# Optimization experiments

Hardware: AMD Instinct MI355X
Metric: run time of the kernel (lower is better)

The kernel has to match this reference:

```python
import jax, jax.numpy as jnp
import numpy as np

B, C, H, W = 1024, 1024, 14, 14
A = 8          # adt_num (number of expert branches)
CH = C // 4    # expert bottleneck width


def setup_inputs() -> dict:
    key = jax.random.key(0)
    ks = jax.random.split(key, 5)
    s_in = 1.0 / np.sqrt(C)
    s_hid = 1.0 / np.sqrt(CH)
    return {
        "features": jax.random.normal(ks[0], (B, C, H, W), dtype=jnp.float32),
        "fc_w": jax.random.normal(ks[1], (A, C), dtype=jnp.float32) * s_in,
        "fc_b": jnp.zeros((A,), dtype=jnp.float32),
        "fc1_w": jax.random.normal(ks[2], (A, C, CH), dtype=jnp.float32) * s_in,
        "fc1_b": jnp.zeros((A, CH), dtype=jnp.float32),
        "fc2_w": jax.random.normal(ks[3], (A, CH, C), dtype=jnp.float32) * s_hid,
        "fc2_b": jnp.zeros((A, C), dtype=jnp.float32),
    }


def reference(features, fc_w, fc_b, fc1_w, fc1_b, fc2_w, fc2_b):
    # Global average pool over spatial dims: [B, C]
    pooled = jnp.mean(features.reshape(features.shape[0], features.shape[1], -1), axis=2)
    # All adt_num expert branches as one batched GEMM pair: [B, A, CH] -> [B, A, C]
    h = jax.nn.relu(jnp.einsum("bc,ach->bah", pooled, fc1_w) + fc1_b)
    expert = jnp.einsum("bah,ahc->bac", h, fc2_w) + fc2_b
    # Softmax gating over experts: [B, A]
    gate = jax.nn.softmax(pooled @ fc_w.T + fc_b, axis=1)
    # Gate-weighted sum of expert outputs: [B, C]
    mixed = jnp.einsum("ba,bac->bc", gate, expert)
    # Sigmoid channel gate + residual: out = x * sigmoid(mixed) + x
    scale = jax.nn.sigmoid(mixed)[:, :, None, None]
    return features * scale + features
```

## Files before the change

### kernel.cpp

```cpp
#include <hip/hip_runtime.h>

#define B_  1024
#define C_  1024
#define HW_ 196
#define A_  8
#define CH_ 256
#define N1_ 2048
#define K2_ 2048

typedef __attribute__((ext_vector_type(8))) short short8;
typedef __attribute__((ext_vector_type(4))) float f32x4;

#define KT1 32
#define KT2 64

static __device__ __forceinline__ unsigned short f2bf(float x) {
  union { float f; unsigned u; } v; v.f = x;
  unsigned r = (v.u + 0x7FFFu + ((v.u >> 16) & 1u)) >> 16;
  return (unsigned short)r;
}

__global__ __launch_bounds__(256) void pooltc_k(const float* __restrict__ f,
                                                float* __restrict__ pooled,
                                                const float* __restrict__ fc1_w,
                                                const float* __restrict__ fc2_w,
                                                unsigned short* __restrict__ w1t,
                                                unsigned short* __restrict__ w2t) {
  __shared__ float tile[32][33];
  if (blockIdx.x < 4096) {
    unsigned row = blockIdx.x * 256 + threadIdx.x;
    const f32x4* p = (const f32x4*)f + (size_t)row * 49;
    float s = 0.f;
    #pragma unroll 3
    for (int j = 0; j < 12; ++j) {
      f32x4 a = p[4 * j + 0], b = p[4 * j + 1], c = p[4 * j + 2], d = p[4 * j + 3];
      s += (a.x + a.y) + (a.z + a.w);
      s += (b.x + b.y) + (b.z + b.w);
      s += (c.x + c.y) + (c.z + c.w);
      s += (d.x + d.y) + (d.z + d.w);
    }
    f32x4 e = p[48];
    s += (e.x + e.y) + (e.z + e.w);
    pooled[row] = s * (1.0f / 196.0f);
  } else {
    int t = blockIdx.x - 4096;
    const float* in; unsigned short* outb; int Cc, nt0, kt, KT;
    if (t < 2048) {
      int a = t >> 8, rem = t & 255;
      int c0 = (rem & 7) * 32, k0 = (rem >> 3) * 32;
      in  = fc1_w + (size_t)a * (C_ * CH_) + (size_t)k0 * CH_ + c0;
      Cc = CH_;
      nt0 = a * 16 + (c0 >> 4);  kt = k0 >> 5;  KT = KT1;  outb = w1t;
    } else {
      t -= 2048;
      int a = t >> 8, rem = t & 255;
      int c0 = (rem & 31) * 32, ch0 = (rem >> 5) * 32;
      in  = fc2_w + (size_t)a * (CH_ * C_) + (size_t)ch0 * C_ + c0;
      Cc = C_;
      nt0 = c0 >> 4;  kt = a * 8 + (ch0 >> 5);  KT = KT2;  outb = w2t;
    }
    int tx = threadIdx.x & 31, ty = threadIdx.x >> 5;
    #pragma unroll
    for (int i = 0; i < 32; i += 8)
      tile[ty + i][tx] = in[(size_t)(ty + i) * Cc + tx];
    __syncthreads();
    int tt = threadIdx.x;
    if (tt < 128) {
      int ct = tt >> 6, kg = (tt >> 4) & 3, r = tt & 15;
      short8 v;
      #pragma unroll
      for (int j = 0; j < 8; ++j)
        v[j] = (short)f2bf(tile[kg * 8 + j][ct * 16 + r]);
      size_t base = ((size_t)(nt0 + ct) * KT + kt) * 512 + (size_t)(kg * 16 + r) * 8;
      *(short8*)(outb + base) = v;
    }
  }
}

__global__ void gate_k(const float* __restrict__ pooled, const float* __restrict__ fc_w,
                       const float* __restrict__ fc_b, float* __restrict__ gate,
                       unsigned short* __restrict__ a1t) {
  __shared__ float dots[A_];
  if (blockIdx.x < 1024) {
    int b = blockIdx.x;
    int wave = threadIdx.x >> 6, lane = threadIdx.x & 63;
    const float* p = pooled + (size_t)b * C_;
    for (int e = wave; e < A_; e += 4) {
      const float* wrow = fc_w + (size_t)e * C_;
      float sum = 0.f;
      for (int c = lane; c < C_; c += 64) sum += p[c] * wrow[c];
      #pragma unroll
      for (int off = 32; off > 0; off >>= 1) sum += __shfl_down(sum, off, 64);
      if (lane == 0) dots[e] = sum + fc_b[e];
    }
    __syncthreads();
    if (threadIdx.x == 0) {
      float mx = dots[0];
      for (int e = 1; e < A_; ++e) mx = fmaxf(mx, dots[e]);
      float ex[A_], se = 0.f;
      for (int e = 0; e < A_; ++e) { ex[e] = __expf(dots[e] - mx); se += ex[e]; }
      float inv = 1.0f / se;
      for (int e = 0; e < A_; ++e) gate[(size_t)b * A_ + e] = ex[e] * inv;
    }
  } else {
    int h = blockIdx.x - 1024;
    int rt = h >> 1, kt0 = (h & 1) * 16;
    int t = threadIdx.x;
    int e0 = 2 * t;
    int kg = e0 >> 7, r = (e0 >> 3) & 15, j0 = e0 & 7;
    int row = rt * 16 + r;
    for (int kt = kt0; kt < kt0 + 16; ++kt) {
      int col = kt * 32 + kg * 8 + j0;
      float v0 = pooled[(size_t)row * C_ + col];
      float v1 = pooled[(size_t)row * C_ + col + 1];
      size_t base = ((size_t)rt * KT1 + kt) * 512 + e0;
      a1t[base]     = f2bf(v0);
      a1t[base + 1] = f2bf(v1);
    }
  }
}

__global__ __launch_bounds__(256) void gemm1_k(const unsigned short* __restrict__ A1,
                                               const unsigned short* __restrict__ W1,
                                               const float* __restrict__ fc1_b,
                                               const float* __restrict__ gate,
                                               unsigned short* __restrict__ gh) {
  int w = threadIdx.x >> 6, lane = threadIdx.x & 63;
  int rt0 = blockIdx.x * 4 + (w >> 1) * 2;
  int nt0 = blockIdx.y * 4 + (w & 1) * 2;
  const short8* Ap0 = (const short8*)(A1 + (size_t)(rt0    ) * KT1 * 512 + lane * 8);
  const short8* Ap1 = (const short8*)(A1 + (size_t)(rt0 + 1) * KT1 * 512 + lane * 8);
  const short8* Bp0 = (const short8*)(W1 + (size_t)(nt0    ) * KT1 * 512 + lane * 8);
  const short8* Bp1 = (const short8*)(W1 + (size_t)(nt0 + 1) * KT1 * 512 + lane * 8);
  f32x4 acc[2][2];
  acc[0][0] = (f32x4){0,0,0,0}; acc[0][1] = acc[0][0];
  acc[1][0] = acc[0][0];        acc[1][1] = acc[0][0];
  #pragma unroll 4
  for (int kt = 0; kt < KT1; ++kt) {
    short8 a0 = Ap0[64 * kt], a1 = Ap1[64 * kt];
    short8 b0 = Bp0[64 * kt], b1 = Bp1[64 * kt];
    acc[0][0] = __builtin_amdgcn_mfma_f32_16x16x32_bf16(a0, b0, acc[0][0], 0, 0, 0);
    acc[0][1] = __builtin_amdgcn_mfma_f32_16x16x32_bf16(a0, b1, acc[0][1], 0, 0, 0);
    acc[1][0] = __builtin_amdgcn_mfma_f32_16x16x32_bf16(a1, b0, acc[1][0], 0, 0, 0);
    acc[1][1] = __builtin_amdgcn_mfma_f32_16x16x32_bf16(a1, b1, acc[1][1], 0, 0, 0);
  }
  int r = lane & 15, kg = lane >> 4;
  #pragma unroll
  for (int mi = 0; mi < 2; ++mi)
    #pragma unroll
    for (int ni = 0; ni < 2; ++ni) {
      int col = (nt0 + ni) * 16 + r;
      float bias = fc1_b[col];
      int aidx = col >> 8;
      #pragma unroll
      for (int reg = 0; reg < 4; ++reg) {
        int row = (rt0 + mi) * 16 + kg * 4 + reg;
        float val = acc[mi][ni][reg] + bias;
        val = fmaxf(val, 0.f) * gate[row * A_ + aidx];
        size_t idx = ((size_t)(row >> 4) * KT2 + (col >> 5)) * 512
                   + (size_t)((col >> 3) & 3) * 128 + (size_t)(row & 15) * 8 + (col & 7);
        gh[idx] = f2bf(val);
      }
    }
}

__global__ __launch_bounds__(256) void gemm2_k(const unsigned short* __restrict__ GH,
                                               const unsigned short* __restrict__ W2,
                                               const float* __restrict__ gate,
                                               const float* __restrict__ fc2_b,
                                               float* __restrict__ s_out) {
  int w = threadIdx.x >> 6, lane = threadIdx.x & 63;
  int rt0 = blockIdx.x * 4 + (w >> 1) * 2;
  int nt0 = blockIdx.y * 4 + (w & 1) * 2;
  const short8* Ap0 = (const short8*)(GH + (size_t)(rt0    ) * KT2 * 512 + lane * 8);
  const short8* Ap1 = (const short8*)(GH + (size_t)(rt0 + 1) * KT2 * 512 + lane * 8);
  const short8* Bp0 = (const short8*)(W2 + (size_t)(nt0    ) * KT2 * 512 + lane * 8);
  const short8* Bp1 = (const short8*)(W2 + (size_t)(nt0 + 1) * KT2 * 512 + lane * 8);
  f32x4 acc[2][2];
  acc[0][0] = (f32x4){0,0,0,0}; acc[0][1] = acc[0][0];
  acc[1][0] = acc[0][0];        acc[1][1] = acc[0][0];
  #pragma unroll 4
  for (int kt = 0; kt < KT2; ++kt) {
    short8 a0 = Ap0[64 * kt], a1 = Ap1[64 * kt];
    short8 b0 = Bp0[64 * kt], b1 = Bp1[64 * kt];
    acc[0][0] = __builtin_amdgcn_mfma_f32_16x16x32_bf16(a0, b0, acc[0][0], 0, 0, 0);
    acc[0][1] = __builtin_amdgcn_mfma_f32_16x16x32_bf16(a0, b1, acc[0][1], 0, 0, 0);
    acc[1][0] = __builtin_amdgcn_mfma_f32_16x16x32_bf16(a1, b0, acc[1][0], 0, 0, 0);
    acc[1][1] = __builtin_amdgcn_mfma_f32_16x16x32_bf16(a1, b1, acc[1][1], 0, 0, 0);
  }
  int r = lane & 15, kg = lane >> 4;
  #pragma unroll
  for (int mi = 0; mi < 2; ++mi)
    #pragma unroll
    for (int ni = 0; ni < 2; ++ni) {
      int col = (nt0 + ni) * 16 + r;
      float b8[A_];
      #pragma unroll
      for (int a = 0; a < A_; ++a) b8[a] = fc2_b[a * C_ + col];
      #pragma unroll
      for (int reg = 0; reg < 4; ++reg) {
        int row = (rt0 + mi) * 16 + kg * 4 + reg;
        const float* g = gate + (size_t)row * A_;
        float bias = 0.f;
        #pragma unroll
        for (int a = 0; a < A_; ++a) bias += g[a] * b8[a];
        float mixed = acc[mi][ni][reg] + bias;
        s_out[(size_t)row * C_ + col] = 1.0f + 1.0f / (1.0f + __expf(-mixed));
      }
    }
}

__global__ __launch_bounds__(256) void apply_k(const f32x4* __restrict__ f,
                                               const float* __restrict__ s,
                                               f32x4* __restrict__ out, unsigned total4) {
  unsigned i = blockIdx.x * 256 + threadIdx.x;
  unsigned stride = gridDim.x * 256;
  for (; i < total4; i += stride) {
    f32x4 v = __builtin_nontemporal_load(&f[i]);
    float m = s[i / 49u];
    v *= m;
    __builtin_nontemporal_store(v, &out[i]);
  }
}

extern "C" void kernel_launch(void* const* d_in, const int* in_sizes, int n_in,
                              void* d_out, int out_size, void* d_ws, size_t ws_size,
                              hipStream_t stream) {
  const float* features = (const float*)d_in[0];
  const float* fc_w  = (const float*)d_in[1];
  const float* fc_b  = (const float*)d_in[2];
  const float* fc1_w = (const float*)d_in[3];
  const float* fc1_b = (const float*)d_in[4];
  const float* fc2_w = (const float*)d_in[5];
  const float* fc2_b = (const float*)d_in[6];
  float* out = (float*)d_out;
  char* ws = (char*)d_ws;

  float*          pooled = (float*)(ws);
  unsigned short* a1t    = (unsigned short*)(ws + 0x400000);
  float*          gate   = (float*)(ws + 0x600000);
  unsigned short* gh     = (unsigned short*)(ws + 0x610000);
  unsigned short* w1t    = (unsigned short*)(ws + 0xA10000);
  unsigned short* w2t    = (unsigned short*)(ws + 0xE10000);
  float*          s_buf  = (float*)(ws + 0x1210000);

  pooltc_k<<<8192, 256, 0, stream>>>(features, pooled, fc1_w, fc2_w, w1t, w2t);
  gate_k<<<1152, 256, 0, stream>>>(pooled, fc_w, fc_b, gate, a1t);
  gemm1_k<<<dim3(16, 32), 256, 0, stream>>>(a1t, w1t, fc1_b, gate, gh);
  gemm2_k<<<dim3(16, 16), 256, 0, stream>>>(gh, w2t, gate, fc2_b, s_buf);
  apply_k<<<8192, 256, 0, stream>>>((const f32x4*)features, s_buf, (f32x4*)out,
                                    (unsigned)(out_size / 4));
}
```

Baseline: 515.0 us.

## Fuse all stages into one persistent kernel with software grid barriers

Replaces five kernel launches with one persistent kernel of 512 blocks that separates the stages (pool and weight transpose, gating, GEMM1, GEMM2, apply) with atomic-counter grid barriers. The bf16 A-operand layout for GEMM1 is now written directly during pooling, which removes the separate a1t repack pass. The aim is to cut launch gaps and tail effects between stages. In exchange, each stage runs with only 512 blocks, so the streaming pool and apply phases have less latency hiding, and the barriers depend on every block being co-resident.

Result: slower. 1.039 ms (+101.7%).

```diff
diff --git a/kernel.cpp b/kernel.cpp
--- a/kernel.cpp
+++ b/kernel.cpp
@@ -2,17 +2,14 @@
 
 #define B_  1024
 #define C_  1024
-#define HW_ 196
 #define A_  8
 #define CH_ 256
-#define N1_ 2048
-#define K2_ 2048
+#define KT1 32
+#define KT2 64
+#define G_  512
 
 typedef __attribute__((ext_vector_type(8))) short short8;
 typedef __attribute__((ext_vector_type(4))) float f32x4;
-
-#define KT1 32
-#define KT2 64
 
 static __device__ __forceinline__ unsigned short f2bf(float x) {
   union { float f; unsigned u; } v; v.f = x;
@@ -20,70 +17,99 @@
   return (unsigned short)r;
 }
 
-__global__ __launch_bounds__(256) void pooltc_k(const float* __restrict__ f,
-                                                float* __restrict__ pooled,
-                                                const float* __restrict__ fc1_w,
-                                                const float* __restrict__ fc2_w,
-                                                unsigned short* __restrict__ w1t,
-                                                unsigned short* __restrict__ w2t) {
+__device__ unsigned long long g_bar[4];
+
+static __device__ __forceinline__ void gridbar(int slot) {
+  __syncthreads();
+  if (threadIdx.x == 0) {
+    __threadfence();
+    unsigned long long v = __hip_atomic_fetch_add(&g_bar[slot], 1ull,
+                              __ATOMIC_ACQ_REL, __HIP_MEMORY_SCOPE_AGENT) + 1ull;
+    unsigned long long tgt = ((v + (unsigned long long)(G_ - 1)) /
+                              (unsigned long long)G_) * (unsigned long long)G_;
+    while (__hip_atomic_load(&g_bar[slot], __ATOMIC_ACQUIRE,
+                             __HIP_MEMORY_SCOPE_AGENT) < tgt)
+      __builtin_amdgcn_s_sleep(2);
+    __threadfence();
+  }
+  __syncthreads();
+}
+
+
+__global__ __launch_bounds__(256, 2) void fused_k(
+    const float* __restrict__ features,
+    const float* __restrict__ fc_w,  const float* __restrict__ fc_b,
+    const float* __restrict__ fc1_w, const float* __restrict__ fc1_b,
+    const float* __restrict__ fc2_w, const float* __restrict__ fc2_b,
+    float* __restrict__ out,
+    float* __restrict__ pooled, unsigned short* __restrict__ a1t,
+    float* __restrict__ gate,   unsigned short* __restrict__ gh,
+    unsigned short* __restrict__ w1t, unsigned short* __restrict__ w2t,
+    float* __restrict__ s_buf) {
   __shared__ float tile[32][33];
-  if (blockIdx.x < 4096) {
-    unsigned row = blockIdx.x * 256 + threadIdx.x;
-    const f32x4* p = (const f32x4*)f + (size_t)row * 49;
-    float s = 0.f;
-    #pragma unroll 3
-    for (int j = 0; j < 12; ++j) {
-      f32x4 a = p[4 * j + 0], b = p[4 * j + 1], c = p[4 * j + 2], d = p[4 * j + 3];
-      s += (a.x + a.y) + (a.z + a.w);
-      s += (b.x + b.y) + (b.z + b.w);
-      s += (c.x + c.y) + (c.z + c.w);
-      s += (d.x + d.y) + (d.z + d.w);
-    }
-    f32x4 e = p[48];
-    s += (e.x + e.y) + (e.z + e.w);
-    pooled[row] = s * (1.0f / 196.0f);
-  } else {
-    int t = blockIdx.x - 4096;
-    const float* in; unsigned short* outb; int Cc, nt0, kt, KT;
-    if (t < 2048) {
-      int a = t >> 8, rem = t & 255;
-      int c0 = (rem & 7) * 32, k0 = (rem >> 3) * 32;
-      in  = fc1_w + (size_t)a * (C_ * CH_) + (size_t)k0 * CH_ + c0;
-      Cc = CH_;
-      nt0 = a * 16 + (c0 >> 4);  kt = k0 >> 5;  KT = KT1;  outb = w1t;
+  __shared__ float dots[A_];
+  const int bid = blockIdx.x;
+  const int tid = threadIdx.x;
+
+  for (int u = bid; u < 8192; u += G_) {
+    if (u < 4096) {
+      unsigned rowf = (unsigned)u * 256 + tid;
+      const f32x4* p = (const f32x4*)features + (size_t)rowf * 49;
+      float s = 0.f;
+      #pragma unroll 3
+      for (int j = 0; j < 12; ++j) {
+        f32x4 a = p[4 * j + 0], b = p[4 * j + 1], c = p[4 * j + 2], d = p[4 * j + 3];
+        s += (a.x + a.y) + (a.z + a.w);
+        s += (b.x + b.y) + (b.z + b.w);
+        s += (c.x + c.y) + (c.z + c.w);
+        s += (d.x + d.y) + (d.z + d.w);
+      }
+      f32x4 e = p[48];
+      s += (e.x + e.y) + (e.z + e.w);
+      float m = s * (1.0f / 196.0f);
+      pooled[rowf] = m;
+      int b = rowf >> 10, c = rowf & 1023;
+      size_t idx = ((size_t)(b >> 4) * KT1 + (c >> 5)) * 512
+                 + (size_t)((c >> 3) & 3) * 128 + (size_t)(b & 15) * 8 + (c & 7);
+      a1t[idx] = f2bf(m);
     } else {
-      t -= 2048;
-      int a = t >> 8, rem = t & 255;
-      int c0 = (rem & 31) * 32, ch0 = (rem >> 5) * 32;
-      in  = fc2_w + (size_t)a * (CH_ * C_) + (size_t)ch0 * C_ + c0;
-      Cc = C_;
-      nt0 = c0 >> 4;  kt = a * 8 + (ch0 >> 5);  KT = KT2;  outb = w2t;
-    }
-    int tx = threadIdx.x & 31, ty = threadIdx.x >> 5;
-    #pragma unroll
-    for (int i = 0; i < 32; i += 8)
-      tile[ty + i][tx] = in[(size_t)(ty + i) * Cc + tx];
-    __syncthreads();
-    int tt = threadIdx.x;
-    if (tt < 128) {
-      int ct = tt >> 6, kg = (tt >> 4) & 3, r = tt & 15;
-      short8 v;
-      #pragma unroll
-      for (int j = 0; j < 8; ++j)
-        v[j] = (short)f2bf(tile[kg * 8 + j][ct * 16 + r]);
-      size_t base = ((size_t)(nt0 + ct) * KT + kt) * 512 + (size_t)(kg * 16 + r) * 8;
-      *(short8*)(outb + base) = v;
-    }
-  }
-}
-
-__global__ void gate_k(const float* __restrict__ pooled, const float* __restrict__ fc_w,
-                       const float* __restrict__ fc_b, float* __restrict__ gate,
-                       unsigned short* __restrict__ a1t) {
-  __shared__ float dots[A_];
-  if (blockIdx.x < 1024) {
-    int b = blockIdx.x;
-    int wave = threadIdx.x >> 6, lane = threadIdx.x & 63;
+      int t = u - 4096;
+      const float* in; unsigned short* outb; int Cc, nt0, kt, KT;
+      if (t < 2048) {
+        int a = t >> 8, rem = t & 255;
+        int c0 = (rem & 7) * 32, k0 = (rem >> 3) * 32;
+        in  = fc1_w + (size_t)a * (C_ * CH_) + (size_t)k0 * CH_ + c0;
+        Cc = CH_;
+        nt0 = a * 16 + (c0 >> 4);  kt = k0 >> 5;  KT = KT1;  outb = w1t;
+      } else {
+        t -= 2048;
+        int a = t >> 8, rem = t & 255;
+        int c0 = (rem & 31) * 32, ch0 = (rem >> 5) * 32;
+        in  = fc2_w + (size_t)a * (CH_ * C_) + (size_t)ch0 * C_ + c0;
+        Cc = C_;
+        nt0 = c0 >> 4;  kt = a * 8 + (ch0 >> 5);  KT = KT2;  outb = w2t;
+      }
+      int tx = tid & 31, ty = tid >> 5;
+      #pragma unroll
+      for (int i = 0; i < 32; i += 8)
+        tile[ty + i][tx] = in[(size_t)(ty + i) * Cc + tx];
+      __syncthreads();
+      if (tid < 128) {
+        int ct = tid >> 6, kg = (tid >> 4) & 3, r = tid & 15;
+        short8 v;
+        #pragma unroll
+        for (int j = 0; j < 8; ++j)
+          v[j] = (short)f2bf(tile[kg * 8 + j][ct * 16 + r]);
+        size_t base = ((size_t)(nt0 + ct) * KT + kt) * 512 + (size_t)(kg * 16 + r) * 8;
+        *(short8*)(outb + base) = v;
+      }
+      __syncthreads();
+    }
+  }
+  gridbar(0);
+
+  for (int b = bid; b < B_; b += G_) {
+    int wave = tid >> 6, lane = tid & 63;
     const float* p = pooled + (size_t)b * C_;
     for (int e = wave; e < A_; e += 4) {
       const float* wrow = fc_w + (size_t)e * C_;
@@ -94,7 +120,7 @@
       if (lane == 0) dots[e] = sum + fc_b[e];
     }
     __syncthreads();
-    if (threadIdx.x == 0) {
+    if (tid == 0) {
       float mx = dots[0];
       for (int e = 1; e < A_; ++e) mx = fmaxf(mx, dots[e]);
       float ex[A_], se = 0.f;
@@ -102,124 +128,114 @@
       float inv = 1.0f / se;
       for (int e = 0; e < A_; ++e) gate[(size_t)b * A_ + e] = ex[e] * inv;
     }
-  } else {
-    int h = blockIdx.x - 1024;
-    int rt = h >> 1, kt0 = (h & 1) * 16;
-    int t = threadIdx.x;
-    int e0 = 2 * t;
-    int kg = e0 >> 7, r = (e0 >> 3) & 15, j0 = e0 & 7;
-    int row = rt * 16 + r;
-    for (int kt = kt0; kt < kt0 + 16; ++kt) {
-      int col = kt * 32 + kg * 8 + j0;
-      float v0 = pooled[(size_t)row * C_ + col];
-      float v1 = pooled[(size_t)row * C_ + col + 1];
-      size_t base = ((size_t)rt * KT1 + kt) * 512 + e0;
-      a1t[base]     = f2bf(v0);
-      a1t[base + 1] = f2bf(v1);
-    }
-  }
-}
-
-__global__ __launch_bounds__(256) void gemm1_k(const unsigned short* __restrict__ A1,
-                                               const unsigned short* __restrict__ W1,
-                                               const float* __restrict__ fc1_b,
-                                               const float* __restrict__ gate,
-                                               unsigned short* __restrict__ gh) {
-  int w = threadIdx.x >> 6, lane = threadIdx.x & 63;
-  int rt0 = blockIdx.x * 4 + (w >> 1) * 2;
-  int nt0 = blockIdx.y * 4 + (w & 1) * 2;
-  const short8* Ap0 = (const short8*)(A1 + (size_t)(rt0    ) * KT1 * 512 + lane * 8);
-  const short8* Ap1 = (const short8*)(A1 + (size_t)(rt0 + 1) * KT1 * 512 + lane * 8);
-  const short8* Bp0 = (const short8*)(W1 + (size_t)(nt0    ) * KT1 * 512 + lane * 8);
-  const short8* Bp1 = (const short8*)(W1 + (size_t)(nt0 + 1) * KT1 * 512 + lane * 8);
-  f32x4 acc[2][2];
-  acc[0][0] = (f32x4){0,0,0,0}; acc[0][1] = acc[0][0];
-  acc[1][0] = acc[0][0];        acc[1][1] = acc[0][0];
-  #pragma unroll 4
-  for (int kt = 0; kt < KT1; ++kt) {
-    short8 a0 = Ap0[64 * kt], a1 = Ap1[64 * kt];
-    short8 b0 = Bp0[64 * kt], b1 = Bp1[64 * kt];
-    acc[0][0] = __builtin_amdgcn_mfma_f32_16x16x32_bf16(a0, b0, acc[0][0], 0, 0, 0);
-    acc[0][1] = __builtin_amdgcn_mfma_f32_16x16x32_bf16(a0, b1, acc[0][1], 0, 0, 0);
-    acc[1][0] = __builtin_amdgcn_mfma_f32_16x16x32_bf16(a1, b0, acc[1][0], 0, 0, 0);
-    acc[1][1] = __builtin_amdgcn_mfma_f32_16x16x32_bf16(a1, b1, acc[1][1], 0, 0, 0);
-  }
-  int r = lane & 15, kg = lane >> 4;
-  #pragma unroll
-  for (int mi = 0; mi < 2; ++mi)
+    __syncthreads();
+  }
+  gridbar(1);
+
+  {
+    int bx = bid >> 5, by = bid & 31;
+    int w = tid >> 6, lane = tid & 63;
+    int rt0 = bx * 4 + (w >> 1) * 2;
+    int nt0 = by * 4 + (w & 1) * 2;
+    const short8* Ap0 = (const short8*)(a1t + (size_t)(rt0    ) * KT1 * 512 + lane * 8);
+    const short8* Ap1 = (const short8*)(a1t + (size_t)(rt0 + 1) * KT1 * 512 + lane * 8);
+    const short8* Bp0 = (const short8*)(w1t + (size_t)(nt0    ) * KT1 * 512 + lane * 8);
+    const short8* Bp1 = (const short8*)(w1t + (size_t)(nt0 + 1) * KT1 * 512 + lane * 8);
+    f32x4 acc[2][2];
+    acc[0][0] = (f32x4){0,0,0,0}; acc[0][1] = acc[0][0];
+    acc[1][0] = acc[0][0];        acc[1][1] = acc[0][0];
+    #pragma unroll 4
+    for (int kt = 0; kt < KT1; ++kt) {
+      short8 a0 = Ap0[64 * kt], a1 = Ap1[64 * kt];
+      short8 b0 = Bp0[64 * kt], b1 = Bp1[64 * kt];
+      acc[0][0] = __builtin_amdgcn_mfma_f32_16x16x32_bf16(a0, b0, acc[0][0], 0, 0, 0);
+      acc[0][1] = __builtin_amdgcn_mfma_f32_16x16x32_bf16(a0, b1, acc[0][1], 0, 0, 0);
+      acc[1][0] = __builtin_amdgcn_mfma_f32_16x16x32_bf16(a1, b0, acc[1][0], 0, 0, 0);
+      acc[1][1] = __builtin_amdgcn_mfma_f32_16x16x32_bf16(a1, b1, acc[1][1], 0, 0, 0);
+    }
+    int r = lane & 15, kg = lane >> 4;
     #pragma unroll
-    for (int ni = 0; ni < 2; ++ni) {
-      int col = (nt0 + ni) * 16 + r;
-      float bias = fc1_b[col];
-      int aidx = col >> 8;
-      #pragma unroll
-      for (int reg = 0; reg < 4; ++reg) {
-        int row = (rt0 + mi) * 16 + kg * 4 + reg;
-        float val = acc[mi][ni][reg] + bias;
-        val = fmaxf(val, 0.f) * gate[row * A_ + aidx];
-        size_t idx = ((size_t)(row >> 4) * KT2 + (col >> 5)) * 512
-                   + (size_t)((col >> 3) & 3) * 128 + (size_t)(row & 15) * 8 + (col & 7);
-        gh[idx] = f2bf(val);
-      }
-    }
-}
-
-__global__ __launch_bounds__(256) void gemm2_k(const unsigned short* __restrict__ GH,
-                                               const unsigned short* __restrict__ W2,
-                                               const float* __restrict__ gate,
-                                               const float* __restrict__ fc2_b,
-                                               float* __restrict__ s_out) {
-  int w = threadIdx.x >> 6, lane = threadIdx.x & 63;
-  int rt0 = blockIdx.x * 4 + (w >> 1) * 2;
-  int nt0 = blockIdx.y * 4 + (w & 1) * 2;
-  const short8* Ap0 = (const short8*)(GH + (size_t)(rt0    ) * KT2 * 512 + lane * 8);
-  const short8* Ap1 = (const short8*)(GH + (size_t)(rt0 + 1) * KT2 * 512 + lane * 8);
-  const short8* Bp0 = (const short8*)(W2 + (size_t)(nt0    ) * KT2 * 512 + lane * 8);
-  const short8* Bp1 = (const short8*)(W2 + (size_t)(nt0 + 1) * KT2 * 512 + lane * 8);
-  f32x4 acc[2][2];
-  acc[0][0] = (f32x4){0,0,0,0}; acc[0][1] = acc[0][0];
-  acc[1][0] = acc[0][0];        acc[1][1] = acc[0][0];
-  #pragma unroll 4
-  for (int kt = 0; kt < KT2; ++kt) {
-    short8 a0 = Ap0[64 * kt], a1 = Ap1[64 * kt];
-    short8 b0 = Bp0[64 * kt], b1 = Bp1[64 * kt];
-    acc[0][0] = __builtin_amdgcn_mfma_f32_16x16x32_bf16(a0, b0, acc[0][0], 0, 0, 0);
-    acc[0][1] = __builtin_amdgcn_mfma_f32_16x16x32_bf16(a0, b1, acc[0][1], 0, 0, 0);
-    acc[1][0] = __builtin_amdgcn_mfma_f32_16x16x32_bf16(a1, b0, acc[1][0], 0, 0, 0);
-    acc[1][1] = __builtin_amdgcn_mfma_f32_16x16x32_bf16(a1, b1, acc[1][1], 0, 0, 0);
-  }
-  int r = lane & 15, kg = lane >> 4;
-  #pragma unroll
-  for (int mi = 0; mi < 2; ++mi)
+    for (int mi = 0; mi < 2; ++mi)
+      #pragma unroll
+      for (int ni = 0; ni < 2; ++ni) {
+        int col = (nt0 + ni) * 16 + r;
+        float bias = fc1_b[col];
+        int aidx = col >> 8;
+        #pragma unroll
+        for (int reg = 0; reg < 4; ++reg) {
+          int row = (rt0 + mi) * 16 + kg * 4 + reg;
+          float val = acc[mi][ni][reg] + bias;
+          val = fmaxf(val, 0.f) * gate[row * A_ + aidx];
+          size_t idx = ((size_t)(row >> 4) * KT2 + (col >> 5)) * 512
+                     + (size_t)((col >> 3) & 3) * 128 + (size_t)(row & 15) * 8 + (col & 7);
+          gh[idx] = f2bf(val);
+        }
+      }
+  }
+  gridbar(2);
+
+  if (bid < 256) {
+    int bx = bid >> 4, by = bid & 15;
+    int w = tid >> 6, lane = tid & 63;
+    int rt0 = bx * 4 + (w >> 1) * 2;
+    int nt0 = by * 4 + (w & 1) * 2;
+    const short8* Ap0 = (const short8*)(gh  + (size_t)(rt0    ) * KT2 * 512 + lane * 8);
+    const short8* Ap1 = (const short8*)(gh  + (size_t)(rt0 + 1) * KT2 * 512 + lane * 8);
+    const short8* Bp0 = (const short8*)(w2t + (size_t)(nt0    ) * KT2 * 512 + lane * 8);
+    const short8* Bp1 = (const short8*)(w2t + (size_t)(nt0 + 1) * KT2 * 512 + lane * 8);
+    f32x4 acc[2][2];
+    acc[0][0] = (f32x4){0,0,0,0}; acc[0][1] = acc[0][0];
+    acc[1][0] = acc[0][0];        acc[1][1] = acc[0][0];
+    #pragma unroll 4
+    for (int kt = 0; kt < KT2; ++kt) {
+      short8 a0 = Ap0[64 * kt], a1 = Ap1[64 * kt];
+      short8 b0 = Bp0[64 * kt], b1 = Bp1[64 * kt];
+      acc[0][0] = __builtin_amdgcn_mfma_f32_16x16x32_bf16(a0, b0, acc[0][0], 0, 0, 0);
+      acc[0][1] = __builtin_amdgcn_mfma_f32_16x16x32_bf16(a0, b1, acc[0][1], 0, 0, 0);
+      acc[1][0] = __builtin_amdgcn_mfma_f32_16x16x32_bf16(a1, b0, acc[1][0], 0, 0, 0);
+      acc[1][1] = __builtin_amdgcn_mfma_f32_16x16x32_bf16(a1, b1, acc[1][1], 0, 0, 0);
+    }
+    int r = lane & 15, kg = lane >> 4;
     #pragma unroll
-    for (int ni = 0; ni < 2; ++ni) {
-      int col = (nt0 + ni) * 16 + r;
-      float b8[A_];
-      #pragma unroll
-      for (int a = 0; a < A_; ++a) b8[a] = fc2_b[a * C_ + col];
-      #pragma unroll
-      for (int reg = 0; reg < 4; ++reg) {
-        int row = (rt0 + mi) * 16 + kg * 4 + reg;
-        const float* g = gate + (size_t)row * A_;
-        float bias = 0.f;
-        #pragma unroll
-        for (int a = 0; a < A_; ++a) bias += g[a] * b8[a];
-        float mixed = acc[mi][ni][reg] + bias;
-        s_out[(size_t)row * C_ + col] = 1.0f + 1.0f / (1.0f + __expf(-mixed));
-      }
-    }
-}
-
-__global__ __launch_bounds__(256) void apply_k(const f32x4* __restrict__ f,
-                                               const float* __restrict__ s,
-                                               f32x4* __restrict__ out, unsigned total4) {
-  unsigned i = blockIdx.x * 256 + threadIdx.x;
-  unsigned stride = gridDim.x * 256;
-  for (; i < total4; i += stride) {
-    f32x4 v = __builtin_nontemporal_load(&f[i]);
-    float m = s[i / 49u];
-    v *= m;
-    __builtin_nontemporal_store(v, &out[i]);
+    for (int mi = 0; mi < 2; ++mi)
+      #pragma unroll
+      for (int ni = 0; ni < 2; ++ni) {
+        int col = (nt0 + ni) * 16 + r;
+        float b8[A_];
+        #pragma unroll
+        for (int a = 0; a < A_; ++a) b8[a] = fc2_b[a * C_ + col];
+        #pragma unroll
+        for (int reg = 0; reg < 4; ++reg) {
+          int row = (rt0 + mi) * 16 + kg * 4 + reg;
+          const float* g = gate + (size_t)row * A_;
+          float bias = 0.f;
+          #pragma unroll
+          for (int a = 0; a < A_; ++a) bias += g[a] * b8[a];
+          float mixed = acc[mi][ni][reg] + bias;
+          s_buf[(size_t)row * C_ + col] = 1.0f + 1.0f / (1.0f + __expf(-mixed));
+        }
+      }
+  }
+  gridbar(3);
+
+  {
+    const f32x4* fv = (const f32x4*)features;
+    f32x4* ov = (f32x4*)out;
+    const unsigned stride = G_ * 256;
+    unsigned i0 = (unsigned)bid * 256 + tid;
+    for (int k = 0; k < 49; ++k) {
+      unsigned base = i0 + (unsigned)k * 8u * stride;
+      f32x4 v[8];
+      #pragma unroll
+      for (int m = 0; m < 8; ++m)
+        v[m] = __builtin_nontemporal_load(&fv[base + (unsigned)m * stride]);
+      #pragma unroll
+      for (int m = 0; m < 8; ++m)
+        v[m] *= s_buf[(base + (unsigned)m * stride) / 49u];
+      #pragma unroll
+      for (int m = 0; m < 8; ++m)
+        __builtin_nontemporal_store(v[m], &ov[base + (unsigned)m * stride]);
+    }
   }
 }
 
@@ -244,10 +260,6 @@
   unsigned short* w2t    = (unsigned short*)(ws + 0xE10000);
   float*          s_buf  = (float*)(ws + 0x1210000);
 
-  pooltc_k<<<8192, 256, 0, stream>>>(features, pooled, fc1_w, fc2_w, w1t, w2t);
-  gate_k<<<1152, 256, 0, stream>>>(pooled, fc_w, fc_b, gate, a1t);
-  gemm1_k<<<dim3(16, 32), 256, 0, stream>>>(a1t, w1t, fc1_b, gate, gh);
-  gemm2_k<<<dim3(16, 16), 256, 0, stream>>>(gh, w2t, gate, fc2_b, s_buf);
-  apply_k<<<8192, 256, 0, stream>>>((const f32x4*)features, s_buf, (f32x4*)out,
-                                    (unsigned)(out_size / 4));
-}
+  fused_k<<<G_, 256, 0, stream>>>(features, fc_w, fc_b, fc1_w, fc1_b, fc2_w, fc2_b,
+                                  out, pooled, a1t, gate, gh, w1t, w2t, s_buf);
+}
```
